# Kernel optimization log

Hardware: AMD Instinct MI355X
Metric: run time of the kernel (lower is better)

Reference implementation:

```python
import jax, jax.numpy as jnp
import numpy as np
from jax import lax

DIM = 256          # C
D_INNER = 512      # expand * dim
D_STATE = 16       # N
DT_RANK = 32       # ceil(d_inner / 16)
K_CONV = 4


def setup_inputs() -> dict:
    key = jax.random.key(0)
    ks = jax.random.split(key, 20)
    B, C, H, W = 2, DIM, 64, 64
    Di, N, R = D_INNER, D_STATE, DT_RANK
    s = 0.02
    inp = {
        "decoder_feat": jax.random.normal(ks[0], (B, C, H, W), jnp.float32),
        "encoder_feat": jax.random.normal(ks[1], (B, C, H, W), jnp.float32),
        # CrossMambaFusion params
        "dec_w": jax.random.normal(ks[2], (C, 2 * Di), jnp.float32) * s,
        "dec_b": jnp.zeros((2 * Di,), jnp.float32),
        "enc_w": jax.random.normal(ks[3], (C, Di), jnp.float32) * s,
        "enc_b": jnp.zeros((Di,), jnp.float32),
        "out_w": jax.random.normal(ks[4], (Di, C), jnp.float32) * s,
        "out_b": jnp.zeros((C,), jnp.float32),
        "ln_g": jnp.ones((C,), jnp.float32),
        "ln_b": jnp.zeros((C,), jnp.float32),
        # Mamba block params (inner dim = Di, expand=1.0)
        "in_w": jax.random.normal(ks[5], (Di, 2 * Di), jnp.float32) * s,
        "in_b": jnp.zeros((2 * Di,), jnp.float32),
        "conv_w": jax.random.normal(ks[6], (Di, 1, K_CONV), jnp.float32) * 0.1,
        "conv_b": jnp.zeros((Di,), jnp.float32),
        "x_proj_w": jax.random.normal(ks[7], (Di, R + 2 * N), jnp.float32) * s,
        "dt_w": jax.random.normal(ks[8], (R, Di), jnp.float32) * 0.1,
        "dt_b": jax.random.uniform(ks[9], (Di,), jnp.float32, -4.0, -2.0),  # small dt after softplus
        "A_log": jnp.log(jnp.tile(jnp.arange(1, N + 1, dtype=jnp.float32)[None, :], (Di, 1))),
        "D_param": jnp.ones((Di,), jnp.float32),
        "m_out_w": jax.random.normal(ks[10], (Di, Di), jnp.float32) * s,
        "m_out_b": jnp.zeros((Di,), jnp.float32),
    }
    return inp


def _mamba(x, in_w, in_b, conv_w, conv_b, x_proj_w, dt_w, dt_b, A_log, D_param, m_out_w, m_out_b):
    # x: (B, L, Di)
    Bsz, L, Di = x.shape
    N, R = D_STATE, DT_RANK
    xz = x @ in_w + in_b                      # (B, L, 2*Di)
    xm, z = jnp.split(xz, 2, axis=-1)
    # causal depthwise conv over the sequence axis
    xc = jnp.swapaxes(xm, 1, 2)               # (B, Di, L)
    xc = lax.conv_general_dilated(
        xc, conv_w, window_strides=(1,), padding=[(K_CONV - 1, 0)],
        dimension_numbers=("NCH", "OIH", "NCH"), feature_group_count=Di)
    xc = xc + conv_b[None, :, None]
    u = jax.nn.silu(jnp.swapaxes(xc, 1, 2))   # (B, L, Di)
    x_dbl = u @ x_proj_w                      # (B, L, R+2N)
    dt = jax.nn.softplus(x_dbl[..., :R] @ dt_w + dt_b)   # (B, L, Di)
    Bm = x_dbl[..., R:R + N]                  # (B, L, N)
    Cm = x_dbl[..., R + N:]                   # (B, L, N)
    A = -jnp.exp(A_log)                       # (Di, N)

    def step(h, t):
        dt_t, u_t, B_t, C_t = t               # (B,Di),(B,Di),(B,N),(B,N)
        dA = jnp.exp(dt_t[..., None] * A)     # (B, Di, N)
        h = h * dA + (dt_t * u_t)[..., None] * B_t[:, None, :]
        y = jnp.einsum("bdn,bn->bd", h, C_t)
        return h, y

    h0 = jnp.zeros((Bsz, Di, N), x.dtype)
    _, ys = lax.scan(step, h0, (jnp.swapaxes(dt, 0, 1), jnp.swapaxes(u, 0, 1),
                                jnp.swapaxes(Bm, 0, 1), jnp.swapaxes(Cm, 0, 1)))
    y = jnp.swapaxes(ys, 0, 1) + u * D_param  # skip connection via D
    y = y * jax.nn.silu(z)
    return y @ m_out_w + m_out_b


def reference(decoder_feat, encoder_feat, dec_w, dec_b, enc_w, enc_b, out_w, out_b,
              ln_g, ln_b, in_w, in_b, conv_w, conv_b, x_proj_w, dt_w, dt_b,
              A_log, D_param, m_out_w, m_out_b):
    B, C, H, W = decoder_feat.shape
    Di = D_INNER
    dec = jnp.transpose(decoder_feat, (0, 2, 3, 1)).reshape(B, H * W, C)
    enc = jnp.transpose(encoder_feat, (0, 2, 3, 1)).reshape(B, H * W, C)
    dec_proj = dec @ dec_w + dec_b
    dec_x, dec_gate = dec_proj[..., :Di], dec_proj[..., Di:]
    enc_p = enc @ enc_w + enc_b
    combined = dec_x * jax.nn.sigmoid(enc_p) + enc_p          # (B, L, Di)
    processed = _mamba(combined, in_w, in_b, conv_w, conv_b, x_proj_w,
                       dt_w, dt_b, A_log, D_param, m_out_w, m_out_b)
    out = (processed * jax.nn.sigmoid(dec_gate)) @ out_w + out_b
    res = out + dec
    mu = jnp.mean(res, axis=-1, keepdims=True)
    var = jnp.mean(jnp.square(res - mu), axis=-1, keepdims=True)
    res = (res - mu) * lax.rsqrt(var + 1e-5) * ln_g + ln_b
    return jnp.transpose(res.reshape(B, H, W, C), (0, 3, 1, 2))
```

## Files before the change

kernel.cpp:

```cpp
#include <hip/hip_runtime.h>
#include <hip/hip_bf16.h>

typedef __bf16 bf16x8_t __attribute__((ext_vector_type(8)));
typedef float f32x4_t __attribute__((ext_vector_type(4)));

__device__ __forceinline__ float sigmoidf_(float x) { return 1.0f / (1.0f + __expf(-x)); }
__device__ __forceinline__ float siluf_(float x) { return x * sigmoidf_(x); }
__device__ __forceinline__ float softplusf_(float x) {
    return fmaxf(x, 0.0f) + log1pf(__expf(-fabsf(x)));
}
__device__ __forceinline__ float b2f(ushort u) { return __uint_as_float(((unsigned)u) << 16); }
__device__ __forceinline__ ushort f2b(float f) {
    return (ushort)__bfloat16_as_ushort(__float2bfloat16(f));
}

__global__ __launch_bounds__(256) void k_prep(
    const float* __restrict__ dec_w, const float* __restrict__ enc_w,
    const float* __restrict__ in_w, const float* __restrict__ m_out_w,
    const float* __restrict__ out_w, const float* __restrict__ x_proj_w,
    const float* __restrict__ dt_w,
    const float* __restrict__ dec, const float* __restrict__ enc,
    __hip_bfloat16* __restrict__ dec_wT, __hip_bfloat16* __restrict__ enc_wT,
    __hip_bfloat16* __restrict__ in_wT, __hip_bfloat16* __restrict__ m_out_wT,
    __hip_bfloat16* __restrict__ out_wT, __hip_bfloat16* __restrict__ xpwT,
    __hip_bfloat16* __restrict__ dtwT,
    __hip_bfloat16* __restrict__ decL, __hip_bfloat16* __restrict__ encL)
{
    __shared__ float tile[64][65];
    if (blockIdx.x < 5312) {
        int gid = blockIdx.x * 256 + threadIdx.x;
        const float* src; __hip_bfloat16* dst; int lk, N, idx;
        if (gid < 262144)       { src = dec_w;    dst = dec_wT;   lk = 8; N = 1024; idx = gid; }
        else if (gid < 393216)  { src = enc_w;    dst = enc_wT;   lk = 8; N = 512;  idx = gid - 262144; }
        else if (gid < 917504)  { src = in_w;     dst = in_wT;    lk = 9; N = 1024; idx = gid - 393216; }
        else if (gid < 1179648) { src = m_out_w;  dst = m_out_wT; lk = 9; N = 512;  idx = gid - 917504; }
        else if (gid < 1310720) { src = out_w;    dst = out_wT;   lk = 9; N = 256;  idx = gid - 1179648; }
        else if (gid < 1343488) { src = x_proj_w; dst = xpwT;     lk = 9; N = 64;   idx = gid - 1310720; }
        else                    { src = dt_w;     dst = dtwT;     lk = 5; N = 512;  idx = gid - 1343488; }
        int K = 1 << lk;
        int n = idx >> lk, k = idx & (K - 1);
        dst[idx] = __float2bfloat16(src[(size_t)k * N + n]);
        return;
    }
    const int bid = blockIdx.x - 5312;
    const int t = threadIdx.x;
    const int ct = bid & 3;
    const int lt = (bid >> 2) & 63;
    const int sel = bid >> 8;
    const int b = sel & 1, ten = sel >> 1;
    const float* src = ten ? enc : dec;
    __hip_bfloat16* dst = ten ? encL : decL;
    const size_t ibase = (size_t)b * 256 * 4096 + (size_t)(ct * 64) * 4096 + (size_t)lt * 64;
#pragma unroll
    for (int i = 0; i < 16; ++i) {
        int c = i * 4 + (t >> 6), l = t & 63;
        tile[c][l] = src[ibase + (size_t)c * 4096 + l];
    }
    __syncthreads();
    const size_t obase = ((size_t)b * 4096 + (size_t)lt * 64) * 256 + ct * 64;
#pragma unroll
    for (int i = 0; i < 16; ++i) {
        int l = i * 4 + (t >> 6), c = t & 63;
        dst[obase + (size_t)l * 256 + c] = __float2bfloat16(tile[c][l]);
    }
}

template <int EPI, int K>
__global__ __launch_bounds__(256) void bgemm(
    const __hip_bfloat16* __restrict__ A, const __hip_bfloat16* __restrict__ Bt,
    const float* __restrict__ bias, void* __restrict__ out0,
    void* __restrict__ out1, const void* __restrict__ extra)
{
    __shared__ ushort At[128 * 32];
    __shared__ ushort Bl[128 * 32];
    const int tid = threadIdx.x;
    const int wave = tid >> 6, lane = tid & 63;
    const int n0 = blockIdx.x * 128, m0 = blockIdx.y * 128;
    const int wm = (wave >> 1) * 64, wn = (wave & 1) * 64;
    f32x4_t acc[4][4] = {};
    const int fr = lane & 15, fq = (lane >> 4) * 8;

    for (int k0 = 0; k0 < K; k0 += 32) {
#pragma unroll
        for (int q = 0; q < 2; ++q) {
            int idx = q * 256 + tid;
            int row = idx >> 2, ch = (idx & 3) * 8;
            uint4 va = *(const uint4*)&A[(size_t)(m0 + row) * K + k0 + ch];
            uint4 vb = *(const uint4*)&Bt[(size_t)(n0 + row) * K + k0 + ch];
            *(uint4*)&At[row * 32 + ch] = va;
            *(uint4*)&Bl[row * 32 + ch] = vb;
        }
        __syncthreads();
        bf16x8_t af[4], bf[4];
#pragma unroll
        for (int i = 0; i < 4; ++i) {
            af[i] = *(bf16x8_t*)&At[(wm + i * 16 + fr) * 32 + fq];
            bf[i] = *(bf16x8_t*)&Bl[(wn + i * 16 + fr) * 32 + fq];
        }
#pragma unroll
        for (int i = 0; i < 4; ++i)
#pragma unroll
            for (int j = 0; j < 4; ++j)
                acc[i][j] = __builtin_amdgcn_mfma_f32_16x16x32_bf16(af[i], bf[j], acc[i][j], 0, 0, 0);
        __syncthreads();
    }

    const int col = lane & 15, rbase = (lane >> 4) * 4;
#pragma unroll
    for (int i = 0; i < 4; ++i) {
#pragma unroll
        for (int j = 0; j < 4; ++j) {
#pragma unroll
            for (int r = 0; r < 4; ++r) {
                int m = m0 + wm + i * 16 + rbase + r;
                int n = n0 + wn + j * 16 + col;
                float v = acc[i][j][r] + bias[n];
                if (EPI == 0) {
                    ((__hip_bfloat16*)out0)[(size_t)m * 512 + n] = __float2bfloat16(v);
                } else if (EPI == 2) {
                    if (n < 512)
                        ((__hip_bfloat16*)out0)[(size_t)m * 512 + n] = __float2bfloat16(v);
                    else
                        ((__hip_bfloat16*)out1)[(size_t)m * 512 + (n - 512)] =
                            __float2bfloat16(siluf_(v));
                } else {
                    float g = __bfloat162float(((const __hip_bfloat16*)extra)[(size_t)m * 512 + n]);
                    ((__hip_bfloat16*)out0)[(size_t)m * 512 + n] = __float2bfloat16(v * g);
                }
            }
        }
    }
}

__global__ __launch_bounds__(256) void k_dec_enc(
    const __hip_bfloat16* __restrict__ decL, const __hip_bfloat16* __restrict__ encL,
    const __hip_bfloat16* __restrict__ dec_wT, const __hip_bfloat16* __restrict__ enc_wT,
    const float* __restrict__ dec_b, const float* __restrict__ enc_b,
    __hip_bfloat16* __restrict__ combined, __hip_bfloat16* __restrict__ gate_sig)
{
    __shared__ __align__(16) ushort At[128 * 32];
    __shared__ __align__(16) ushort Bl[128 * 32];
    const int tid = threadIdx.x;
    const int wave = tid >> 6, lane = tid & 63;
    const int n0 = blockIdx.x * 128, m0 = blockIdx.y * 128;
    const int wm = (wave >> 1) * 64, wn = (wave & 1) * 64;
    const int fr = lane & 15, fq = (lane >> 4) * 8;
    const int col = lane & 15, rbase = (lane >> 4) * 4;

    f32x4_t accD[4][4] = {};
    for (int k0 = 0; k0 < 256; k0 += 32) {
#pragma unroll
        for (int q = 0; q < 2; ++q) {
            int idx = q * 256 + tid;
            int row = idx >> 2, ch = (idx & 3) * 8;
            uint4 va = *(const uint4*)&decL[(size_t)(m0 + row) * 256 + k0 + ch];
            uint4 vb = *(const uint4*)&dec_wT[(size_t)(n0 + row) * 256 + k0 + ch];
            *(uint4*)&At[row * 32 + ch] = va;
            *(uint4*)&Bl[row * 32 + ch] = vb;
        }
        __syncthreads();
        bf16x8_t af[4], bf[4];
#pragma unroll
        for (int i = 0; i < 4; ++i) {
            af[i] = *(bf16x8_t*)&At[(wm + i * 16 + fr) * 32 + fq];
            bf[i] = *(bf16x8_t*)&Bl[(wn + i * 16 + fr) * 32 + fq];
        }
#pragma unroll
        for (int i = 0; i < 4; ++i)
#pragma unroll
            for (int j = 0; j < 4; ++j)
                accD[i][j] = __builtin_amdgcn_mfma_f32_16x16x32_bf16(af[i], bf[j], accD[i][j], 0, 0, 0);
        __syncthreads();
    }

    if (n0 < 512) {
        f32x4_t accE[4][4] = {};
        for (int k0 = 0; k0 < 256; k0 += 32) {
#pragma unroll
            for (int q = 0; q < 2; ++q) {
                int idx = q * 256 + tid;
                int row = idx >> 2, ch = (idx & 3) * 8;
                uint4 va = *(const uint4*)&encL[(size_t)(m0 + row) * 256 + k0 + ch];
                uint4 vb = *(const uint4*)&enc_wT[(size_t)(n0 + row) * 256 + k0 + ch];
                *(uint4*)&At[row * 32 + ch] = va;
                *(uint4*)&Bl[row * 32 + ch] = vb;
            }
            __syncthreads();
            bf16x8_t af[4], bf[4];
#pragma unroll
            for (int i = 0; i < 4; ++i) {
                af[i] = *(bf16x8_t*)&At[(wm + i * 16 + fr) * 32 + fq];
                bf[i] = *(bf16x8_t*)&Bl[(wn + i * 16 + fr) * 32 + fq];
            }
#pragma unroll
            for (int i = 0; i < 4; ++i)
#pragma unroll
                for (int j = 0; j < 4; ++j)
                    accE[i][j] = __builtin_amdgcn_mfma_f32_16x16x32_bf16(af[i], bf[j], accE[i][j], 0, 0, 0);
            __syncthreads();
        }
#pragma unroll
        for (int i = 0; i < 4; ++i)
#pragma unroll
            for (int j = 0; j < 4; ++j)
#pragma unroll
                for (int r = 0; r < 4; ++r) {
                    int m = m0 + wm + i * 16 + rbase + r;
                    int n = n0 + wn + j * 16 + col;
                    float ep = accE[i][j][r] + enc_b[n];
                    float v = accD[i][j][r] + dec_b[n];
                    combined[(size_t)m * 512 + n] =
                        __float2bfloat16(fmaf(v, sigmoidf_(ep), ep));
                }
    } else {
#pragma unroll
        for (int i = 0; i < 4; ++i)
#pragma unroll
            for (int j = 0; j < 4; ++j)
#pragma unroll
                for (int r = 0; r < 4; ++r) {
                    int m = m0 + wm + i * 16 + rbase + r;
                    int n = n0 + wn + j * 16 + col;
                    float v = accD[i][j][r] + dec_b[n];
                    gate_sig[(size_t)m * 512 + (n - 512)] = __float2bfloat16(sigmoidf_(v));
                }
    }
}

#define CHUNK 16
#define NCHUNK 256

__global__ __launch_bounds__(512) void k_conv_scan(
    const __hip_bfloat16* __restrict__ xm, const float* __restrict__ conv_w,
    const float* __restrict__ conv_b, const __hip_bfloat16* __restrict__ xpwT,
    const __hip_bfloat16* __restrict__ dtwT, const float* __restrict__ dt_b,
    const float* __restrict__ A_log,
    __hip_bfloat16* __restrict__ u_out, float* __restrict__ Bm,
    float* __restrict__ Cm, __hip_bfloat16* __restrict__ dt_out,
    float* __restrict__ hpart, float* __restrict__ dtsums)
{
    __shared__ __align__(16) ushort us_dts[CHUNK][512 + 8];
    __shared__ __align__(16) ushort adt[CHUNK][32 + 8];
    __shared__ float BsL[CHUNK * 16];
    const int tid = threadIdx.x;
    const int wave = tid >> 6, lane = tid & 63;
    const int bl0 = blockIdx.x * CHUNK;
    const int l0 = bl0 & 4095;
    const int b = blockIdx.x >> 8;
    const int chunk = blockIdx.x & (NCHUNK - 1);
    const int fr = lane & 15, fq = (lane >> 4) * 8;
    const int col = lane & 15, rbase = (lane >> 4) * 4;

    float uarr[CHUNK];
    {
        const int d = tid;
        const float cw0 = conv_w[d * 4], cw1 = conv_w[d * 4 + 1];
        const float cw2 = conv_w[d * 4 + 2], cw3 = conv_w[d * 4 + 3];
        const float cb = conv_b[d];
        const ushort* xs = (const ushort*)xm;
        float x0 = (l0 >= 3) ? b2f(xs[(size_t)(bl0 - 3) * 512 + d]) : 0.f;
        float x1 = (l0 >= 2) ? b2f(xs[(size_t)(bl0 - 2) * 512 + d]) : 0.f;
        float x2 = (l0 >= 1) ? b2f(xs[(size_t)(bl0 - 1) * 512 + d]) : 0.f;
#pragma unroll
        for (int t = 0; t < CHUNK; ++t) {
            float x3 = b2f(xs[(size_t)(bl0 + t) * 512 + d]);
            float a = cb;
            a = fmaf(cw0, x0, a);
            a = fmaf(cw1, x1, a);
            a = fmaf(cw2, x2, a);
            a = fmaf(cw3, x3, a);
            float uv = siluf_(a);
            uarr[t] = uv;
            ushort ub = f2b(uv);
            us_dts[t][d] = ub;
            ((ushort*)u_out)[(size_t)(bl0 + t) * 512 + d] = ub;
            x0 = x1; x1 = x2; x2 = x3;
        }
    }
    __syncthreads();

    if (wave < 4) {
        const int n0w = wave * 16;
        f32x4_t acc = {};
        const __hip_bfloat16* bp = xpwT + (size_t)(n0w + fr) * 512;
#pragma unroll
        for (int k0 = 0; k0 < 512; k0 += 32) {
            bf16x8_t af = *(bf16x8_t*)&us_dts[fr][k0 + fq];
            bf16x8_t bf = *(const bf16x8_t*)&bp[k0 + fq];
            acc = __builtin_amdgcn_mfma_f32_16x16x32_bf16(af, bf, acc, 0, 0, 0);
        }
#pragma unroll
        for (int r = 0; r < 4; ++r) {
            int m = rbase + r;
            int n = n0w + col;
            float v = acc[r];
            if (n < 32) {
                adt[m][n] = f2b(v);
            } else if (n < 48) {
                BsL[m * 16 + (n - 32)] = v;
                Bm[(size_t)(bl0 + m) * 16 + (n - 32)] = v;
            } else {
                Cm[(size_t)(bl0 + m) * 16 + (n - 48)] = v;
            }
        }
    }
    __syncthreads();

    {
        bf16x8_t af = *(bf16x8_t*)&adt[fr][fq];
#pragma unroll
        for (int t = 0; t < 4; ++t) {
            int nt = wave * 4 + t;
            bf16x8_t bf = *(const bf16x8_t*)&dtwT[(size_t)(nt * 16 + fr) * 32 + fq];
            f32x4_t acc = {};
            acc = __builtin_amdgcn_mfma_f32_16x16x32_bf16(af, bf, acc, 0, 0, 0);
#pragma unroll
            for (int r = 0; r < 4; ++r) {
                int m = rbase + r;
                int n = nt * 16 + col;
                ushort dv = f2b(softplusf_(acc[r] + dt_b[n]));
                us_dts[m][n] = dv;
                ((ushort*)dt_out)[(size_t)(bl0 + m) * 512 + n] = dv;
            }
        }
    }
    __syncthreads();

    {
        const int d = tid;
        float Av[16];
#pragma unroll
        for (int n = 0; n < 16; n += 4) {
            float4 al = *(const float4*)&A_log[d * 16 + n];
            Av[n + 0] = -__expf(al.x);
            Av[n + 1] = -__expf(al.y);
            Av[n + 2] = -__expf(al.z);
            Av[n + 3] = -__expf(al.w);
        }
        float h[16] = {};
        float dtsum = 0.f;
#pragma unroll
        for (int t = 0; t < CHUNK; ++t) {
            float dtv = b2f(us_dts[t][d]);
            float dtu = dtv * uarr[t];
            dtsum += dtv;
            const float* Bt = &BsL[t * 16];
#pragma unroll
            for (int n = 0; n < 16; ++n)
                h[n] = fmaf(h[n], __expf(dtv * Av[n]), dtu * Bt[n]);
        }
        const size_t sidx = ((size_t)b * NCHUNK + chunk) * 512 + d;
        const size_t idx = sidx * 16;
#pragma unroll
        for (int n = 0; n < 16; n += 4)
            *(float4*)&hpart[idx + n] = make_float4(h[n], h[n + 1], h[n + 2], h[n + 3]);
        dtsums[sidx] = dtsum;
    }
}

__global__ __launch_bounds__(128) void k_scan_comb(
    const float* __restrict__ hpart, const float* __restrict__ dtsums,
    const float* __restrict__ A_log, float* __restrict__ h_in)
{
    const int gid = blockIdx.x * 128 + threadIdx.x;
    const int n = gid & 15;
    const int d = (gid >> 4) & 511;
    const int b = gid >> 13;
    const float Av = -__expf(A_log[d * 16 + n]);
    const size_t base = (size_t)b * NCHUNK;
    float h = 0.f;
    for (int c0 = 0; c0 < NCHUNK; c0 += 16) {
        float hp[16], ef[16];
#pragma unroll
        for (int u = 0; u < 16; ++u) {
            const size_t sidx = (base + c0 + u) * 512 + d;
            hp[u] = hpart[sidx * 16 + n];
            ef[u] = dtsums[sidx];
        }
#pragma unroll
        for (int u = 0; u < 16; ++u)
            ef[u] = __expf(Av * ef[u]);
#pragma unroll
        for (int u = 0; u < 16; ++u) {
            const size_t sidx = (base + c0 + u) * 512 + d;
            h_in[sidx * 16 + n] = h;
            h = fmaf(h, ef[u], hp[u]);
        }
    }
}

__global__ __launch_bounds__(512) void k_scan_fin(
    const __hip_bfloat16* __restrict__ dt, const __hip_bfloat16* __restrict__ u,
    const float* __restrict__ Bmp, const float* __restrict__ Cmp,
    const float* __restrict__ A_log, const float* __restrict__ Dp,
    const __hip_bfloat16* __restrict__ zs, const float* __restrict__ h_in,
    __hip_bfloat16* __restrict__ yout)
{
    __shared__ float Bs[CHUNK * 16];
    __shared__ float Cs[CHUNK * 16];
    const int d = threadIdx.x;
    const int chunk = blockIdx.x & (NCHUNK - 1);
    const int b = blockIdx.x >> 8;
    const size_t row0 = (size_t)b * 4096 + (size_t)chunk * CHUNK;

    if (d < CHUNK * 16) {
        Bs[d] = Bmp[row0 * 16 + d];
        Cs[d] = Cmp[row0 * 16 + d];
    }
    float Av[16];
#pragma unroll
    for (int n = 0; n < 16; n += 4) {
        float4 al = *(const float4*)&A_log[d * 16 + n];
        Av[n + 0] = -__expf(al.x);
        Av[n + 1] = -__expf(al.y);
        Av[n + 2] = -__expf(al.z);
        Av[n + 3] = -__expf(al.w);
    }
    const float Dv = Dp[d];
    float h[16];
    const size_t idx = (((size_t)b * NCHUNK + chunk) * 512 + d) * 16;
#pragma unroll
    for (int n = 0; n < 16; n += 4) {
        float4 hv = *(const float4*)&h_in[idx + n];
        h[n] = hv.x; h[n + 1] = hv.y; h[n + 2] = hv.z; h[n + 3] = hv.w;
    }
    __syncthreads();

    const ushort* dtp = (const ushort*)dt + row0 * 512 + d;
    const ushort* up = (const ushort*)u + row0 * 512 + d;
    const ushort* zp = (const ushort*)zs + row0 * 512 + d;
    __hip_bfloat16* yp = yout + row0 * 512 + d;
#pragma unroll
    for (int t = 0; t < CHUNK; ++t) {
        float dtv = b2f(dtp[(size_t)t * 512]);
        float uv = b2f(up[(size_t)t * 512]);
        float zv = b2f(zp[(size_t)t * 512]);
        float dtu = dtv * uv;
        const float* Bt = &Bs[t * 16];
        const float* Ct = &Cs[t * 16];
        float y = 0.f;
#pragma unroll
        for (int n = 0; n < 16; ++n) {
            h[n] = fmaf(h[n], __expf(dtv * Av[n]), dtu * Bt[n]);
            y = fmaf(h[n], Ct[n], y);
        }
        yp[(size_t)t * 512] = __float2bfloat16((y + uv * Dv) * zv);
    }
}

__global__ __launch_bounds__(256) void k_mout_ln(
    const __hip_bfloat16* __restrict__ Y, const __hip_bfloat16* __restrict__ mwT,
    const float* __restrict__ m_out_b, const __hip_bfloat16* __restrict__ gate,
    const __hip_bfloat16* __restrict__ owT, const float* __restrict__ out_b,
    const __hip_bfloat16* __restrict__ decL,
    const float* __restrict__ ln_g, const float* __restrict__ ln_b,
    float* __restrict__ outp)
{
    __shared__ __align__(16) ushort Gs[32][520];
    __shared__ __align__(16) ushort At[32 * 32];
    __shared__ __align__(16) ushort Bl[512 * 32];
    __shared__ float red[4][32][2];
    __shared__ float lmu[32], lsc[32];
    const int tid = threadIdx.x;
    const int wave = tid >> 6, lane = tid & 63;
    const int m0 = blockIdx.x * 32;
    const int fr = lane & 15, fq = (lane >> 4) * 8;
    const int col = lane & 15, rbase = (lane >> 4) * 4;

#pragma unroll
    for (int q = 0; q < 8; ++q) {
        int idx = q * 256 + tid;
        int row = idx >> 6, ch = (idx & 63) * 8;
        *(uint4*)&Gs[row][ch] = *(const uint4*)&gate[(size_t)(m0 + row) * 512 + ch];
    }

    const int wn1 = wave * 128;
    f32x4_t acc1[2][8] = {};
    for (int k0 = 0; k0 < 512; k0 += 32) {
        if (tid < 128) {
            int row = tid >> 2, ch = (tid & 3) * 8;
            *(uint4*)&At[row * 32 + ch] = *(const uint4*)&Y[(size_t)(m0 + row) * 512 + k0 + ch];
        }
#pragma unroll
        for (int q = 0; q < 8; ++q) {
            int idx = q * 256 + tid;
            int row = idx >> 2, ch = (idx & 3) * 8;
            *(uint4*)&Bl[row * 32 + ch] = *(const uint4*)&mwT[(size_t)row * 512 + k0 + ch];
        }
        __syncthreads();
        bf16x8_t af[2], bf[8];
#pragma unroll
        for (int i = 0; i < 2; ++i)
            af[i] = *(bf16x8_t*)&At[(i * 16 + fr) * 32 + fq];
#pragma unroll
        for (int j = 0; j < 8; ++j)
            bf[j] = *(bf16x8_t*)&Bl[(wn1 + j * 16 + fr) * 32 + fq];
#pragma unroll
        for (int i = 0; i < 2; ++i)
#pragma unroll
            for (int j = 0; j < 8; ++j)
                acc1[i][j] = __builtin_amdgcn_mfma_f32_16x16x32_bf16(af[i], bf[j], acc1[i][j], 0, 0, 0);
        __syncthreads();
    }
#pragma unroll
    for (int i = 0; i < 2; ++i)
#pragma unroll
        for (int j = 0; j < 8; ++j)
#pragma unroll
            for (int r = 0; r < 4; ++r) {
                int m = i * 16 + rbase + r;
                int n = wn1 + j * 16 + col;
                float g = b2f(Gs[m][n]);
                Gs[m][n] = f2b((acc1[i][j][r] + m_out_b[n]) * g);
            }
    __syncthreads();

    const int wn2 = wave * 64;
    f32x4_t acc2[2][4] = {};
    for (int k0 = 0; k0 < 512; k0 += 32) {
#pragma unroll
        for (int q = 0; q < 4; ++q) {
            int idx = q * 256 + tid;
            int row = idx >> 2, ch = (idx & 3) * 8;
            *(uint4*)&Bl[row * 32 + ch] = *(const uint4*)&owT[(size_t)row * 512 + k0 + ch];
        }
        __syncthreads();
        bf16x8_t af[2], bf[4];
#pragma unroll
        for (int i = 0; i < 2; ++i)
            af[i] = *(bf16x8_t*)&Gs[i * 16 + fr][k0 + fq];
#pragma unroll
        for (int j = 0; j < 4; ++j)
            bf[j] = *(bf16x8_t*)&Bl[(wn2 + j * 16 + fr) * 32 + fq];
#pragma unroll
        for (int i = 0; i < 2; ++i)
#pragma unroll
            for (int j = 0; j < 4; ++j)
                acc2[i][j] = __builtin_amdgcn_mfma_f32_16x16x32_bf16(af[i], bf[j], acc2[i][j], 0, 0, 0);
        __syncthreads();
    }

#pragma unroll
    for (int i = 0; i < 2; ++i) {
#pragma unroll
        for (int r = 0; r < 4; ++r) {
            int ml = i * 16 + rbase + r;
            int m = m0 + ml;
            float s = 0.f, sq = 0.f;
#pragma unroll
            for (int j = 0; j < 4; ++j) {
                int n = wn2 + j * 16 + col;
                float dv = b2f(((const ushort*)decL)[(size_t)m * 256 + n]);
                float v = acc2[i][j][r] + out_b[n] + dv;
                acc2[i][j][r] = v;
                s += v;
                sq = fmaf(v, v, sq);
            }
            s += __shfl_xor(s, 1);  sq += __shfl_xor(sq, 1);
            s += __shfl_xor(s, 2);  sq += __shfl_xor(sq, 2);
            s += __shfl_xor(s, 4);  sq += __shfl_xor(sq, 4);
            s += __shfl_xor(s, 8);  sq += __shfl_xor(sq, 8);
            if (col == 0) { red[wave][ml][0] = s; red[wave][ml][1] = sq; }
        }
    }
    __syncthreads();
    if (tid < 32) {
        float s  = red[0][tid][0] + red[1][tid][0] + red[2][tid][0] + red[3][tid][0];
        float sq = red[0][tid][1] + red[1][tid][1] + red[2][tid][1] + red[3][tid][1];
        float mu = s * (1.0f / 256.0f);
        float var = sq * (1.0f / 256.0f) - mu * mu;
        lmu[tid] = mu;
        lsc[tid] = rsqrtf(var + 1e-5f);
    }
    __syncthreads();
    const int bb = m0 >> 12;
    const int lpos0 = m0 & 4095;
#pragma unroll
    for (int i = 0; i < 2; ++i) {
#pragma unroll
        for (int r = 0; r < 4; ++r) {
            int ml = i * 16 + rbase + r;
            float mu = lmu[ml], sc = lsc[ml];
#pragma unroll
            for (int j = 0; j < 4; ++j) {
                int n = wn2 + j * 16 + col;
                float v = (acc2[i][j][r] - mu) * sc * ln_g[n] + ln_b[n];
                outp[(size_t)bb * (256 * 4096) + (size_t)n * 4096 + lpos0 + ml] = v;
            }
        }
    }
}

extern "C" void kernel_launch(void* const* d_in, const int* in_sizes, int n_in,
                              void* d_out, int out_size, void* d_ws, size_t ws_size,
                              hipStream_t stream)
{
    const float* decoder_feat = (const float*)d_in[0];
    const float* encoder_feat = (const float*)d_in[1];
    const float* dec_w = (const float*)d_in[2];
    const float* dec_b = (const float*)d_in[3];
    const float* enc_w = (const float*)d_in[4];
    const float* enc_b = (const float*)d_in[5];
    const float* out_w = (const float*)d_in[6];
    const float* out_b = (const float*)d_in[7];
    const float* ln_g = (const float*)d_in[8];
    const float* ln_bb = (const float*)d_in[9];
    const float* in_w = (const float*)d_in[10];
    const float* in_b = (const float*)d_in[11];
    const float* conv_w = (const float*)d_in[12];
    const float* conv_b = (const float*)d_in[13];
    const float* x_proj_w = (const float*)d_in[14];
    const float* dt_w = (const float*)d_in[15];
    const float* dt_b = (const float*)d_in[16];
    const float* A_log = (const float*)d_in[17];
    const float* D_param = (const float*)d_in[18];
    const float* m_out_w = (const float*)d_in[19];
    const float* m_out_b = (const float*)d_in[20];

    float* outp = (float*)d_out;
    char* ws = (char*)d_ws;
    const size_t MB = 1024ull * 1024;
    __hip_bfloat16* decL     = (__hip_bfloat16*)(ws + 0 * MB);
    __hip_bfloat16* encL     = (__hip_bfloat16*)(ws + 4 * MB);
    __hip_bfloat16* dec_wT   = (__hip_bfloat16*)(ws + 8 * MB);
    __hip_bfloat16* enc_wT   = (__hip_bfloat16*)(ws + 9 * MB);
    __hip_bfloat16* in_wT    = (__hip_bfloat16*)(ws + 10 * MB);
    __hip_bfloat16* m_out_wT = (__hip_bfloat16*)(ws + 11 * MB);
    __hip_bfloat16* out_wT   = (__hip_bfloat16*)(ws + 12 * MB);
    __hip_bfloat16* xpwT     = (__hip_bfloat16*)(ws + 12 * MB + 262144);
    __hip_bfloat16* dtwT     = (__hip_bfloat16*)(ws + 12 * MB + 262144 + 65536);
    __hip_bfloat16* combined = (__hip_bfloat16*)(ws + 29 * MB);
    __hip_bfloat16* gate_sig = (__hip_bfloat16*)(ws + 37 * MB);
    __hip_bfloat16* xm       = (__hip_bfloat16*)(ws + 45 * MB);
    __hip_bfloat16* z_silu   = (__hip_bfloat16*)(ws + 53 * MB);
    __hip_bfloat16* u_buf    = (__hip_bfloat16*)(ws + 61 * MB);
    __hip_bfloat16* dt_buf   = (__hip_bfloat16*)(ws + 69 * MB);
    float* h_in              = (float*)(ws + 77 * MB);
    float* Bm                = (float*)(ws + 93 * MB);
    float* Cm                = (float*)(ws + 93 * MB + 524288);
    float* dtsums            = (float*)(ws + 94 * MB);
    float* hpart = (float*)(ws + 13 * MB);
    __hip_bfloat16* y_buf = combined;

    k_prep<<<6336, 256, 0, stream>>>(
        dec_w, enc_w, in_w, m_out_w, out_w, x_proj_w, dt_w,
        decoder_feat, encoder_feat,
        dec_wT, enc_wT, in_wT, m_out_wT, out_wT, xpwT, dtwT, decL, encL);
    k_dec_enc<<<dim3(8, 64), 256, 0, stream>>>(
        decL, encL, dec_wT, enc_wT, dec_b, enc_b, combined, gate_sig);
    bgemm<2, 512><<<dim3(8, 64), 256, 0, stream>>>(
        combined, in_wT, in_b, xm, z_silu, nullptr);
    k_conv_scan<<<2 * NCHUNK, 512, 0, stream>>>(
        xm, conv_w, conv_b, xpwT, dtwT, dt_b, A_log,
        u_buf, Bm, Cm, dt_buf, hpart, dtsums);
    k_scan_comb<<<128, 128, 0, stream>>>(hpart, dtsums, A_log, h_in);
    k_scan_fin<<<2 * NCHUNK, 512, 0, stream>>>(
        dt_buf, u_buf, Bm, Cm, A_log, D_param, z_silu, h_in, y_buf);
    k_mout_ln<<<256, 256, 0, stream>>>(
        y_buf, m_out_wT, m_out_b, gate_sig, out_wT, out_b, decL, ln_g, ln_bb, outp);
}
```

Measured before the change: 264.9 us.

## Fuse scan finalization into m_out/LN kernel and tile weight transposes

The chunked scan finalization (k_scan_fin) is folded into k_mout_ln. Each 32-row block now recomputes its two 16-row chunks' y values directly into LDS, which removes the y_buf global round trip and one kernel launch. Weight transposes in k_prep switch from strided per-element gathers to 64x64 LDS-tiled transposes with coalesced reads and writes, so the grid shrinks to far fewer blocks. The gate multiply moves from an LDS preload to a direct global read in the epilogue, and the unused EPI gate path is removed. In exchange, the scan in k_mout_ln runs on only 256 blocks with a serial loop per thread, which may lengthen that kernel.

```diff
diff --git a/kernel.cpp b/kernel.cpp
--- a/kernel.cpp
+++ b/kernel.cpp
@@ -27,23 +27,42 @@
     __hip_bfloat16* __restrict__ decL, __hip_bfloat16* __restrict__ encL)
 {
     __shared__ float tile[64][65];
-    if (blockIdx.x < 5312) {
-        int gid = blockIdx.x * 256 + threadIdx.x;
-        const float* src; __hip_bfloat16* dst; int lk, N, idx;
-        if (gid < 262144)       { src = dec_w;    dst = dec_wT;   lk = 8; N = 1024; idx = gid; }
-        else if (gid < 393216)  { src = enc_w;    dst = enc_wT;   lk = 8; N = 512;  idx = gid - 262144; }
-        else if (gid < 917504)  { src = in_w;     dst = in_wT;    lk = 9; N = 1024; idx = gid - 393216; }
-        else if (gid < 1179648) { src = m_out_w;  dst = m_out_wT; lk = 9; N = 512;  idx = gid - 917504; }
-        else if (gid < 1310720) { src = out_w;    dst = out_wT;   lk = 9; N = 256;  idx = gid - 1179648; }
-        else if (gid < 1343488) { src = x_proj_w; dst = xpwT;     lk = 9; N = 64;   idx = gid - 1310720; }
-        else                    { src = dt_w;     dst = dtwT;     lk = 5; N = 512;  idx = gid - 1343488; }
-        int K = 1 << lk;
-        int n = idx >> lk, k = idx & (K - 1);
-        dst[idx] = __float2bfloat16(src[(size_t)k * N + n]);
+    const int t = threadIdx.x;
+    if (blockIdx.x < 320) {
+        const int bt = blockIdx.x;
+        const float* src; __hip_bfloat16* dst; int K, N, ln2, tt;
+        if (bt < 64)       { src = dec_w;   dst = dec_wT;   K = 256; N = 1024; ln2 = 4; tt = bt; }
+        else if (bt < 96)  { src = enc_w;   dst = enc_wT;   K = 256; N = 512;  ln2 = 3; tt = bt - 64; }
+        else if (bt < 224) { src = in_w;    dst = in_wT;    K = 512; N = 1024; ln2 = 4; tt = bt - 96; }
+        else if (bt < 288) { src = m_out_w; dst = m_out_wT; K = 512; N = 512;  ln2 = 3; tt = bt - 224; }
+        else               { src = out_w;   dst = out_wT;   K = 512; N = 256;  ln2 = 2; tt = bt - 288; }
+        const int k0 = (tt >> ln2) * 64, n0 = (tt & ((1 << ln2) - 1)) * 64;
+#pragma unroll
+        for (int i = 0; i < 16; ++i) {
+            int r = i * 4 + (t >> 6), c = t & 63;
+            tile[r][c] = src[(size_t)(k0 + r) * N + n0 + c];
+        }
+        __syncthreads();
+#pragma unroll
+        for (int i = 0; i < 16; ++i) {
+            int nr = i * 4 + (t >> 6), kc = t & 63;
+            dst[(size_t)(n0 + nr) * K + k0 + kc] = __float2bfloat16(tile[kc][nr]);
+        }
         return;
     }
-    const int bid = blockIdx.x - 5312;
-    const int t = threadIdx.x;
+    if (blockIdx.x < 512) {
+        int gid = (blockIdx.x - 320) * 256 + t;
+        if (gid < 32768) {
+            int n = gid >> 9, k = gid & 511;
+            xpwT[gid] = __float2bfloat16(x_proj_w[(size_t)k * 64 + n]);
+        } else {
+            int idx = gid - 32768;
+            int n = idx >> 5, k = idx & 31;
+            dtwT[idx] = __float2bfloat16(dt_w[(size_t)k * 512 + n]);
+        }
+        return;
+    }
+    const int bid = blockIdx.x - 512;
     const int ct = bid & 3;
     const int lt = (bid >> 2) & 63;
     const int sel = bid >> 8;
@@ -115,17 +134,14 @@
                 int m = m0 + wm + i * 16 + rbase + r;
                 int n = n0 + wn + j * 16 + col;
                 float v = acc[i][j][r] + bias[n];
-                if (EPI == 0) {
-                    ((__hip_bfloat16*)out0)[(size_t)m * 512 + n] = __float2bfloat16(v);
-                } else if (EPI == 2) {
+                if (EPI == 2) {
                     if (n < 512)
                         ((__hip_bfloat16*)out0)[(size_t)m * 512 + n] = __float2bfloat16(v);
                     else
                         ((__hip_bfloat16*)out1)[(size_t)m * 512 + (n - 512)] =
                             __float2bfloat16(siluf_(v));
                 } else {
-                    float g = __bfloat162float(((const __hip_bfloat16*)extra)[(size_t)m * 512 + n]);
-                    ((__hip_bfloat16*)out0)[(size_t)m * 512 + n] = __float2bfloat16(v * g);
+                    ((__hip_bfloat16*)out0)[(size_t)m * 512 + n] = __float2bfloat16(v);
                 }
             }
         }
@@ -389,76 +405,21 @@
     }
 }
 
-__global__ __launch_bounds__(512) void k_scan_fin(
+__global__ __launch_bounds__(256) void k_mout_ln(
     const __hip_bfloat16* __restrict__ dt, const __hip_bfloat16* __restrict__ u,
     const float* __restrict__ Bmp, const float* __restrict__ Cmp,
     const float* __restrict__ A_log, const float* __restrict__ Dp,
     const __hip_bfloat16* __restrict__ zs, const float* __restrict__ h_in,
-    __hip_bfloat16* __restrict__ yout)
-{
-    __shared__ float Bs[CHUNK * 16];
-    __shared__ float Cs[CHUNK * 16];
-    const int d = threadIdx.x;
-    const int chunk = blockIdx.x & (NCHUNK - 1);
-    const int b = blockIdx.x >> 8;
-    const size_t row0 = (size_t)b * 4096 + (size_t)chunk * CHUNK;
-
-    if (d < CHUNK * 16) {
-        Bs[d] = Bmp[row0 * 16 + d];
-        Cs[d] = Cmp[row0 * 16 + d];
-    }
-    float Av[16];
-#pragma unroll
-    for (int n = 0; n < 16; n += 4) {
-        float4 al = *(const float4*)&A_log[d * 16 + n];
-        Av[n + 0] = -__expf(al.x);
-        Av[n + 1] = -__expf(al.y);
-        Av[n + 2] = -__expf(al.z);
-        Av[n + 3] = -__expf(al.w);
-    }
-    const float Dv = Dp[d];
-    float h[16];
-    const size_t idx = (((size_t)b * NCHUNK + chunk) * 512 + d) * 16;
-#pragma unroll
-    for (int n = 0; n < 16; n += 4) {
-        float4 hv = *(const float4*)&h_in[idx + n];
-        h[n] = hv.x; h[n + 1] = hv.y; h[n + 2] = hv.z; h[n + 3] = hv.w;
-    }
-    __syncthreads();
-
-    const ushort* dtp = (const ushort*)dt + row0 * 512 + d;
-    const ushort* up = (const ushort*)u + row0 * 512 + d;
-    const ushort* zp = (const ushort*)zs + row0 * 512 + d;
-    __hip_bfloat16* yp = yout + row0 * 512 + d;
-#pragma unroll
-    for (int t = 0; t < CHUNK; ++t) {
-        float dtv = b2f(dtp[(size_t)t * 512]);
-        float uv = b2f(up[(size_t)t * 512]);
-        float zv = b2f(zp[(size_t)t * 512]);
-        float dtu = dtv * uv;
-        const float* Bt = &Bs[t * 16];
-        const float* Ct = &Cs[t * 16];
-        float y = 0.f;
-#pragma unroll
-        for (int n = 0; n < 16; ++n) {
-            h[n] = fmaf(h[n], __expf(dtv * Av[n]), dtu * Bt[n]);
-            y = fmaf(h[n], Ct[n], y);
-        }
-        yp[(size_t)t * 512] = __float2bfloat16((y + uv * Dv) * zv);
-    }
-}
-
-__global__ __launch_bounds__(256) void k_mout_ln(
-    const __hip_bfloat16* __restrict__ Y, const __hip_bfloat16* __restrict__ mwT,
-    const float* __restrict__ m_out_b, const __hip_bfloat16* __restrict__ gate,
+    const __hip_bfloat16* __restrict__ mwT, const float* __restrict__ m_out_b,
+    const __hip_bfloat16* __restrict__ gate,
     const __hip_bfloat16* __restrict__ owT, const float* __restrict__ out_b,
     const __hip_bfloat16* __restrict__ decL,
     const float* __restrict__ ln_g, const float* __restrict__ ln_b,
     float* __restrict__ outp)
 {
-    __shared__ __align__(16) ushort Gs[32][520];
-    __shared__ __align__(16) ushort At[32 * 32];
+    __shared__ __align__(16) ushort Ys[32][520];
     __shared__ __align__(16) ushort Bl[512 * 32];
+    __shared__ float BCs[2][2][16][16];
     __shared__ float red[4][32][2];
     __shared__ float lmu[32], lsc[32];
     const int tid = threadIdx.x;
@@ -468,19 +429,63 @@
     const int col = lane & 15, rbase = (lane >> 4) * 4;
 
 #pragma unroll
-    for (int q = 0; q < 8; ++q) {
+    for (int q = 0; q < 2; ++q) {
         int idx = q * 256 + tid;
-        int row = idx >> 6, ch = (idx & 63) * 8;
-        *(uint4*)&Gs[row][ch] = *(const uint4*)&gate[(size_t)(m0 + row) * 512 + ch];
-    }
+        int row = idx >> 4, n = idx & 15;
+        BCs[0][row >> 4][row & 15][n] = Bmp[(size_t)(m0 + row) * 16 + n];
+        BCs[1][row >> 4][row & 15][n] = Cmp[(size_t)(m0 + row) * 16 + n];
+    }
+    __syncthreads();
+
+    const int g0 = m0 >> 4;
+#pragma unroll 1
+    for (int c2 = 0; c2 < 2; ++c2) {
+#pragma unroll 1
+        for (int dh = 0; dh < 2; ++dh) {
+            const int d = dh * 256 + tid;
+            const int g = g0 + c2;
+            float Av[16];
+#pragma unroll
+            for (int n = 0; n < 16; n += 4) {
+                float4 al = *(const float4*)&A_log[d * 16 + n];
+                Av[n + 0] = -__expf(al.x);
+                Av[n + 1] = -__expf(al.y);
+                Av[n + 2] = -__expf(al.z);
+                Av[n + 3] = -__expf(al.w);
+            }
+            const float Dv = Dp[d];
+            float h[16];
+            const size_t hidx = ((size_t)g * 512 + d) * 16;
+#pragma unroll
+            for (int n = 0; n < 16; n += 4) {
+                float4 hv = *(const float4*)&h_in[hidx + n];
+                h[n] = hv.x; h[n + 1] = hv.y; h[n + 2] = hv.z; h[n + 3] = hv.w;
+            }
+            const size_t row0 = (size_t)g * 16;
+            const ushort* dtp = (const ushort*)dt + row0 * 512 + d;
+            const ushort* up  = (const ushort*)u  + row0 * 512 + d;
+            const ushort* zp  = (const ushort*)zs + row0 * 512 + d;
+#pragma unroll
+            for (int t = 0; t < 16; ++t) {
+                float dtv = b2f(dtp[(size_t)t * 512]);
+                float uv  = b2f(up[(size_t)t * 512]);
+                float zv  = b2f(zp[(size_t)t * 512]);
+                float dtu = dtv * uv;
+                float y = 0.f;
+#pragma unroll
+                for (int n = 0; n < 16; ++n) {
+                    h[n] = fmaf(h[n], __expf(dtv * Av[n]), dtu * BCs[0][c2][t][n]);
+                    y = fmaf(h[n], BCs[1][c2][t][n], y);
+                }
+                Ys[c2 * 16 + t][d] = f2b((y + uv * Dv) * zv);
+            }
+        }
+    }
+    __syncthreads();
 
     const int wn1 = wave * 128;
     f32x4_t acc1[2][8] = {};
     for (int k0 = 0; k0 < 512; k0 += 32) {
-        if (tid < 128) {
-            int row = tid >> 2, ch = (tid & 3) * 8;
-            *(uint4*)&At[row * 32 + ch] = *(const uint4*)&Y[(size_t)(m0 + row) * 512 + k0 + ch];
-        }
 #pragma unroll
         for (int q = 0; q < 8; ++q) {
             int idx = q * 256 + tid;
@@ -491,7 +496,7 @@
         bf16x8_t af[2], bf[8];
 #pragma unroll
         for (int i = 0; i < 2; ++i)
-            af[i] = *(bf16x8_t*)&At[(i * 16 + fr) * 32 + fq];
+            af[i] = *(bf16x8_t*)&Ys[i * 16 + fr][k0 + fq];
 #pragma unroll
         for (int j = 0; j < 8; ++j)
             bf[j] = *(bf16x8_t*)&Bl[(wn1 + j * 16 + fr) * 32 + fq];
@@ -508,10 +513,10 @@
         for (int j = 0; j < 8; ++j)
 #pragma unroll
             for (int r = 0; r < 4; ++r) {
-                int m = i * 16 + rbase + r;
+                int ml = i * 16 + rbase + r;
                 int n = wn1 + j * 16 + col;
-                float g = b2f(Gs[m][n]);
-                Gs[m][n] = f2b((acc1[i][j][r] + m_out_b[n]) * g);
+                float gv = b2f(((const ushort*)gate)[(size_t)(m0 + ml) * 512 + n]);
+                Ys[ml][n] = f2b((acc1[i][j][r] + m_out_b[n]) * gv);
             }
     __syncthreads();
 
@@ -528,7 +533,7 @@
         bf16x8_t af[2], bf[4];
 #pragma unroll
         for (int i = 0; i < 2; ++i)
-            af[i] = *(bf16x8_t*)&Gs[i * 16 + fr][k0 + fq];
+            af[i] = *(bf16x8_t*)&Ys[i * 16 + fr][k0 + fq];
 #pragma unroll
         for (int j = 0; j < 4; ++j)
             bf[j] = *(bf16x8_t*)&Bl[(wn2 + j * 16 + fr) * 32 + fq];
@@ -639,10 +644,9 @@
     float* Bm                = (float*)(ws + 93 * MB);
     float* Cm                = (float*)(ws + 93 * MB + 524288);
     float* dtsums            = (float*)(ws + 94 * MB);
-    float* hpart = (float*)(ws + 13 * MB);
-    __hip_bfloat16* y_buf = combined;
-
-    k_prep<<<6336, 256, 0, stream>>>(
+    float* hpart             = (float*)(ws + 13 * MB);
+
+    k_prep<<<1536, 256, 0, stream>>>(
         dec_w, enc_w, in_w, m_out_w, out_w, x_proj_w, dt_w,
         decoder_feat, encoder_feat,
         dec_wT, enc_wT, in_wT, m_out_wT, out_wT, xpwT, dtwT, decL, encL);
@@ -654,8 +658,7 @@
         xm, conv_w, conv_b, xpwT, dtwT, dt_b, A_log,
         u_buf, Bm, Cm, dt_buf, hpart, dtsums);
     k_scan_comb<<<128, 128, 0, stream>>>(hpart, dtsums, A_log, h_in);
-    k_scan_fin<<<2 * NCHUNK, 512, 0, stream>>>(
-        dt_buf, u_buf, Bm, Cm, A_log, D_param, z_silu, h_in, y_buf);
     k_mout_ln<<<256, 256, 0, stream>>>(
-        y_buf, m_out_wT, m_out_b, gate_sig, out_wT, out_b, decL, ln_g, ln_bb, outp);
-}
+        dt_buf, u_buf, Bm, Cm, A_log, D_param, z_silu, h_in,
+        m_out_wT, m_out_b, gate_sig, out_wT, out_b, decL, ln_g, ln_bb, outp);
+}
```

Result: slower. 289.3 us (+9.2%).

## Tile weight transposes through LDS and double waves in fused out-projection+LN kernel

Applied to the files above, without the earlier changes.

The elementwise strided weight transpose in the prep kernel is replaced by 64x64 shared-memory tiled transposes, so global reads and writes are coalesced. The small x_proj and dt weights keep a simple path, and the grid shrinks accordingly. The final m_out/out-projection/LayerNorm kernel moves from 4 to 8 waves per block, halving each wave's accumulator tile to raise parallelism and cut register pressure, at the cost of more LDS reduction partials. An unused gate-multiply epilogue variant in bgemm is also simplified.

```diff
diff --git a/kernel.cpp b/kernel.cpp
--- a/kernel.cpp
+++ b/kernel.cpp
@@ -27,23 +27,42 @@
     __hip_bfloat16* __restrict__ decL, __hip_bfloat16* __restrict__ encL)
 {
     __shared__ float tile[64][65];
-    if (blockIdx.x < 5312) {
-        int gid = blockIdx.x * 256 + threadIdx.x;
-        const float* src; __hip_bfloat16* dst; int lk, N, idx;
-        if (gid < 262144)       { src = dec_w;    dst = dec_wT;   lk = 8; N = 1024; idx = gid; }
-        else if (gid < 393216)  { src = enc_w;    dst = enc_wT;   lk = 8; N = 512;  idx = gid - 262144; }
-        else if (gid < 917504)  { src = in_w;     dst = in_wT;    lk = 9; N = 1024; idx = gid - 393216; }
-        else if (gid < 1179648) { src = m_out_w;  dst = m_out_wT; lk = 9; N = 512;  idx = gid - 917504; }
-        else if (gid < 1310720) { src = out_w;    dst = out_wT;   lk = 9; N = 256;  idx = gid - 1179648; }
-        else if (gid < 1343488) { src = x_proj_w; dst = xpwT;     lk = 9; N = 64;   idx = gid - 1310720; }
-        else                    { src = dt_w;     dst = dtwT;     lk = 5; N = 512;  idx = gid - 1343488; }
-        int K = 1 << lk;
-        int n = idx >> lk, k = idx & (K - 1);
-        dst[idx] = __float2bfloat16(src[(size_t)k * N + n]);
+    const int t = threadIdx.x;
+    if (blockIdx.x < 320) {
+        const int bt = blockIdx.x;
+        const float* src; __hip_bfloat16* dst; int K, N, ln2, tt;
+        if (bt < 64)       { src = dec_w;   dst = dec_wT;   K = 256; N = 1024; ln2 = 4; tt = bt; }
+        else if (bt < 96)  { src = enc_w;   dst = enc_wT;   K = 256; N = 512;  ln2 = 3; tt = bt - 64; }
+        else if (bt < 224) { src = in_w;    dst = in_wT;    K = 512; N = 1024; ln2 = 4; tt = bt - 96; }
+        else if (bt < 288) { src = m_out_w; dst = m_out_wT; K = 512; N = 512;  ln2 = 3; tt = bt - 224; }
+        else               { src = out_w;   dst = out_wT;   K = 512; N = 256;  ln2 = 2; tt = bt - 288; }
+        const int k0 = (tt >> ln2) * 64, n0 = (tt & ((1 << ln2) - 1)) * 64;
+#pragma unroll
+        for (int i = 0; i < 16; ++i) {
+            int r = i * 4 + (t >> 6), c = t & 63;
+            tile[r][c] = src[(size_t)(k0 + r) * N + n0 + c];
+        }
+        __syncthreads();
+#pragma unroll
+        for (int i = 0; i < 16; ++i) {
+            int nr = i * 4 + (t >> 6), kc = t & 63;
+            dst[(size_t)(n0 + nr) * K + k0 + kc] = __float2bfloat16(tile[kc][nr]);
+        }
         return;
     }
-    const int bid = blockIdx.x - 5312;
-    const int t = threadIdx.x;
+    if (blockIdx.x < 512) {
+        int gid = (blockIdx.x - 320) * 256 + t;
+        if (gid < 32768) {
+            int n = gid >> 9, k = gid & 511;
+            xpwT[gid] = __float2bfloat16(x_proj_w[(size_t)k * 64 + n]);
+        } else {
+            int idx = gid - 32768;
+            int n = idx >> 5, k = idx & 31;
+            dtwT[idx] = __float2bfloat16(dt_w[(size_t)k * 512 + n]);
+        }
+        return;
+    }
+    const int bid = blockIdx.x - 512;
     const int ct = bid & 3;
     const int lt = (bid >> 2) & 63;
     const int sel = bid >> 8;
@@ -115,17 +134,14 @@
                 int m = m0 + wm + i * 16 + rbase + r;
                 int n = n0 + wn + j * 16 + col;
                 float v = acc[i][j][r] + bias[n];
-                if (EPI == 0) {
-                    ((__hip_bfloat16*)out0)[(size_t)m * 512 + n] = __float2bfloat16(v);
-                } else if (EPI == 2) {
+                if (EPI == 2) {
                     if (n < 512)
                         ((__hip_bfloat16*)out0)[(size_t)m * 512 + n] = __float2bfloat16(v);
                     else
                         ((__hip_bfloat16*)out1)[(size_t)m * 512 + (n - 512)] =
                             __float2bfloat16(siluf_(v));
                 } else {
-                    float g = __bfloat162float(((const __hip_bfloat16*)extra)[(size_t)m * 512 + n]);
-                    ((__hip_bfloat16*)out0)[(size_t)m * 512 + n] = __float2bfloat16(v * g);
+                    ((__hip_bfloat16*)out0)[(size_t)m * 512 + n] = __float2bfloat16(v);
                 }
             }
         }
@@ -448,7 +464,7 @@
     }
 }
 
-__global__ __launch_bounds__(256) void k_mout_ln(
+__global__ __launch_bounds__(512) void k_mout_ln(
     const __hip_bfloat16* __restrict__ Y, const __hip_bfloat16* __restrict__ mwT,
     const float* __restrict__ m_out_b, const __hip_bfloat16* __restrict__ gate,
     const __hip_bfloat16* __restrict__ owT, const float* __restrict__ out_b,
@@ -459,7 +475,7 @@
     __shared__ __align__(16) ushort Gs[32][520];
     __shared__ __align__(16) ushort At[32 * 32];
     __shared__ __align__(16) ushort Bl[512 * 32];
-    __shared__ float red[4][32][2];
+    __shared__ float red[8][32][2];
     __shared__ float lmu[32], lsc[32];
     const int tid = threadIdx.x;
     const int wave = tid >> 6, lane = tid & 63;
@@ -468,44 +484,44 @@
     const int col = lane & 15, rbase = (lane >> 4) * 4;
 
 #pragma unroll
-    for (int q = 0; q < 8; ++q) {
-        int idx = q * 256 + tid;
+    for (int q = 0; q < 4; ++q) {
+        int idx = q * 512 + tid;
         int row = idx >> 6, ch = (idx & 63) * 8;
         *(uint4*)&Gs[row][ch] = *(const uint4*)&gate[(size_t)(m0 + row) * 512 + ch];
     }
 
-    const int wn1 = wave * 128;
-    f32x4_t acc1[2][8] = {};
+    const int wn1 = wave * 64;
+    f32x4_t acc1[2][4] = {};
     for (int k0 = 0; k0 < 512; k0 += 32) {
         if (tid < 128) {
             int row = tid >> 2, ch = (tid & 3) * 8;
             *(uint4*)&At[row * 32 + ch] = *(const uint4*)&Y[(size_t)(m0 + row) * 512 + k0 + ch];
         }
 #pragma unroll
-        for (int q = 0; q < 8; ++q) {
-            int idx = q * 256 + tid;
+        for (int q = 0; q < 4; ++q) {
+            int idx = q * 512 + tid;
             int row = idx >> 2, ch = (idx & 3) * 8;
             *(uint4*)&Bl[row * 32 + ch] = *(const uint4*)&mwT[(size_t)row * 512 + k0 + ch];
         }
         __syncthreads();
-        bf16x8_t af[2], bf[8];
+        bf16x8_t af[2], bf[4];
 #pragma unroll
         for (int i = 0; i < 2; ++i)
             af[i] = *(bf16x8_t*)&At[(i * 16 + fr) * 32 + fq];
 #pragma unroll
-        for (int j = 0; j < 8; ++j)
+        for (int j = 0; j < 4; ++j)
             bf[j] = *(bf16x8_t*)&Bl[(wn1 + j * 16 + fr) * 32 + fq];
 #pragma unroll
         for (int i = 0; i < 2; ++i)
 #pragma unroll
-            for (int j = 0; j < 8; ++j)
+            for (int j = 0; j < 4; ++j)
                 acc1[i][j] = __builtin_amdgcn_mfma_f32_16x16x32_bf16(af[i], bf[j], acc1[i][j], 0, 0, 0);
         __syncthreads();
     }
 #pragma unroll
     for (int i = 0; i < 2; ++i)
 #pragma unroll
-        for (int j = 0; j < 8; ++j)
+        for (int j = 0; j < 4; ++j)
 #pragma unroll
             for (int r = 0; r < 4; ++r) {
                 int m = i * 16 + rbase + r;
@@ -515,27 +531,27 @@
             }
     __syncthreads();
 
-    const int wn2 = wave * 64;
-    f32x4_t acc2[2][4] = {};
+    const int wn2 = wave * 32;
+    f32x4_t acc2[2][2] = {};
     for (int k0 = 0; k0 < 512; k0 += 32) {
 #pragma unroll
-        for (int q = 0; q < 4; ++q) {
-            int idx = q * 256 + tid;
+        for (int q = 0; q < 2; ++q) {
+            int idx = q * 512 + tid;
             int row = idx >> 2, ch = (idx & 3) * 8;
             *(uint4*)&Bl[row * 32 + ch] = *(const uint4*)&owT[(size_t)row * 512 + k0 + ch];
         }
         __syncthreads();
-        bf16x8_t af[2], bf[4];
+        bf16x8_t af[2], bf[2];
 #pragma unroll
         for (int i = 0; i < 2; ++i)
             af[i] = *(bf16x8_t*)&Gs[i * 16 + fr][k0 + fq];
 #pragma unroll
-        for (int j = 0; j < 4; ++j)
+        for (int j = 0; j < 2; ++j)
             bf[j] = *(bf16x8_t*)&Bl[(wn2 + j * 16 + fr) * 32 + fq];
 #pragma unroll
         for (int i = 0; i < 2; ++i)
 #pragma unroll
-            for (int j = 0; j < 4; ++j)
+            for (int j = 0; j < 2; ++j)
                 acc2[i][j] = __builtin_amdgcn_mfma_f32_16x16x32_bf16(af[i], bf[j], acc2[i][j], 0, 0, 0);
         __syncthreads();
     }
@@ -548,7 +564,7 @@
             int m = m0 + ml;
             float s = 0.f, sq = 0.f;
 #pragma unroll
-            for (int j = 0; j < 4; ++j) {
+            for (int j = 0; j < 2; ++j) {
                 int n = wn2 + j * 16 + col;
                 float dv = b2f(((const ushort*)decL)[(size_t)m * 256 + n]);
                 float v = acc2[i][j][r] + out_b[n] + dv;
@@ -565,8 +581,9 @@
     }
     __syncthreads();
     if (tid < 32) {
-        float s  = red[0][tid][0] + red[1][tid][0] + red[2][tid][0] + red[3][tid][0];
-        float sq = red[0][tid][1] + red[1][tid][1] + red[2][tid][1] + red[3][tid][1];
+        float s = 0.f, sq = 0.f;
+#pragma unroll
+        for (int w = 0; w < 8; ++w) { s += red[w][tid][0]; sq += red[w][tid][1]; }
         float mu = s * (1.0f / 256.0f);
         float var = sq * (1.0f / 256.0f) - mu * mu;
         lmu[tid] = mu;
@@ -582,7 +599,7 @@
             int ml = i * 16 + rbase + r;
             float mu = lmu[ml], sc = lsc[ml];
 #pragma unroll
-            for (int j = 0; j < 4; ++j) {
+            for (int j = 0; j < 2; ++j) {
                 int n = wn2 + j * 16 + col;
                 float v = (acc2[i][j][r] - mu) * sc * ln_g[n] + ln_b[n];
                 outp[(size_t)bb * (256 * 4096) + (size_t)n * 4096 + lpos0 + ml] = v;
@@ -639,10 +656,10 @@
     float* Bm                = (float*)(ws + 93 * MB);
     float* Cm                = (float*)(ws + 93 * MB + 524288);
     float* dtsums            = (float*)(ws + 94 * MB);
-    float* hpart = (float*)(ws + 13 * MB);
+    float* hpart             = (float*)(ws + 13 * MB);
     __hip_bfloat16* y_buf = combined;
 
-    k_prep<<<6336, 256, 0, stream>>>(
+    k_prep<<<1536, 256, 0, stream>>>(
         dec_w, enc_w, in_w, m_out_w, out_w, x_proj_w, dt_w,
         decoder_feat, encoder_feat,
         dec_wT, enc_wT, in_wT, m_out_wT, out_wT, xpwT, dtwT, decL, encL);
@@ -656,6 +673,6 @@
     k_scan_comb<<<128, 128, 0, stream>>>(hpart, dtsums, A_log, h_in);
     k_scan_fin<<<2 * NCHUNK, 512, 0, stream>>>(
         dt_buf, u_buf, Bm, Cm, A_log, D_param, z_silu, h_in, y_buf);
-    k_mout_ln<<<256, 256, 0, stream>>>(
+    k_mout_ln<<<256, 512, 0, stream>>>(
         y_buf, m_out_wT, m_out_b, gate_sig, out_wT, out_b, decL, ln_g, ln_bb, outp);
 }
```

Result: faster. 257.1 us (-3.0%).
